# Kernel optimization log

Hardware: AMD Instinct MI355X
Metric: run time of the kernel (lower is better)

## Reference

```python
import jax, jax.numpy as jnp
import numpy as np

N_LVL = 127.0   # 8-bit symmetric: 2**(8-1) - 1
BN_EPS = 1e-5
PATCH = 16


def quant_act(x):
    """Per-tensor 8-bit symmetric quant-dequant (HAWQ-style QuantAct, dynamic range)."""
    scale = jnp.max(jnp.abs(x)) / N_LVL
    xq = jnp.clip(jnp.round(x / scale), -N_LVL, N_LVL) * scale
    return xq, scale


def setup_inputs() -> dict:
    key = jax.random.key(0)
    k0, k1, k2, k3, k4 = jax.random.split(key, 5)
    B, C, H = 128, 3, 224
    dim = 768
    x = jax.random.normal(k0, (B, C, H, H), jnp.float32)
    W = jax.random.normal(k1, (dim, C, PATCH, PATCH), jnp.float32) * 0.02
    b = jax.random.normal(k2, (dim,), jnp.float32) * 0.02
    gamma = jnp.ones((dim,), jnp.float32)
    beta = jnp.zeros((dim,), jnp.float32)
    run_mean = jax.random.normal(k3, (dim,), jnp.float32) * 0.1
    run_var = jax.random.uniform(k4, (dim,), jnp.float32, 0.5, 1.5)
    return {"x": x, "W": W, "b": b, "gamma": gamma, "beta": beta,
            "run_mean": run_mean, "run_var": run_var}


def reference(x, W, b, gamma, beta, run_mean, run_var):
    # --- quant_input ---
    x_q, pre_s = quant_act(x)                                   # [B,3,224,224], scalar
    # --- QuantConv2d: per-out-channel 8-bit symmetric weight quant ---
    w_scale = jnp.max(jnp.abs(W), axis=(1, 2, 3), keepdims=True) / N_LVL  # [dim,1,1,1]
    w_int = jnp.round(W / w_scale)
    x_int = x_q / pre_s                                         # integer-valued activations
    comb_s = w_scale[:, 0, 0, 0] * pre_s                        # [dim] conv output scale
    b_int = jnp.round(b / comb_s)
    y = jax.lax.conv_general_dilated(
        x_int, w_int, window_strides=(PATCH, PATCH), padding='VALID',
        dimension_numbers=('NCHW', 'OIHW', 'NCHW'))             # [B,768,14,14]
    y = (y + b_int[None, :, None, None]) * comb_s[None, :, None, None]
    # --- quant_act_conv ---
    y, _ = quant_act(y)
    # --- GELU (torch nn.GELU default: exact erf) ---
    y = jax.nn.gelu(y, approximate=False)
    # --- qact1 ---
    y, _ = quant_act(y)
    # --- BatchNorm2d (eval mode, running stats) ---
    inv = gamma / jnp.sqrt(run_var + BN_EPS)
    y = y * inv[None, :, None, None] + (beta - run_mean * inv)[None, :, None, None]
    # --- qact2 ---
    y, act_scale = quant_act(y)
    return y, act_scale
```

## Files before the change

### kernel.cpp

```cpp
#include <hip/hip_runtime.h>

#define TOT   19267584
#define MROWS 25088
#define KD    768
#define NPB   196
#define CHW   150528

typedef unsigned int uint;
typedef __attribute__((ext_vector_type(4))) int i32x4;

#define OFF_AQ   0ull
#define OFF_WQ   19267584ull
#define OFF_WSC  19857408ull
#define OFF_INV  19860480ull
#define OFF_SHF  19863552ull
#define OFF_PA   19866624ull
#define OFF_PB   19871328ull
#define OFF_CMN  19876032ull
#define OFF_CMX  19879104ull

__device__ __forceinline__ float wave_max(float v) {
#pragma unroll
  for (int off = 32; off > 0; off >>= 1) v = fmaxf(v, __shfl_xor(v, off));
  return v;
}

__device__ __forceinline__ float block_max(float v) {
  __shared__ float red[4];
  v = wave_max(v);
  __syncthreads();
  if ((threadIdx.x & 63) == 0) red[threadIdx.x >> 6] = v;
  __syncthreads();
  return fmaxf(fmaxf(red[0], red[1]), fmaxf(red[2], red[3]));
}

__global__ void k_maxabs(const float* __restrict__ x, float* __restrict__ pA) {
  const int i0 = blockIdx.x * 256 + threadIdx.x;
  const float4* x4 = (const float4*)x;
  float m = 0.f;
#pragma unroll
  for (int j = 0; j < 16; j += 4) {
    float4 a = x4[i0 + (j + 0) * 301056];
    float4 b = x4[i0 + (j + 1) * 301056];
    float4 c = x4[i0 + (j + 2) * 301056];
    float4 d = x4[i0 + (j + 3) * 301056];
    m = fmaxf(m, fmaxf(fmaxf(fabsf(a.x), fabsf(a.y)), fmaxf(fabsf(a.z), fabsf(a.w))));
    m = fmaxf(m, fmaxf(fmaxf(fabsf(b.x), fabsf(b.y)), fmaxf(fabsf(b.z), fabsf(b.w))));
    m = fmaxf(m, fmaxf(fmaxf(fabsf(c.x), fabsf(c.y)), fmaxf(fabsf(c.z), fabsf(c.w))));
    m = fmaxf(m, fmaxf(fmaxf(fabsf(d.x), fabsf(d.y)), fmaxf(fabsf(d.z), fabsf(d.w))));
  }
  float bm = block_max(m);
  if (threadIdx.x == 0) pA[blockIdx.x] = bm;
}

__global__ void k_wquant(const float* __restrict__ W, const float* __restrict__ gamma,
                         const float* __restrict__ beta, const float* __restrict__ rmean,
                         const float* __restrict__ rvar, signed char* __restrict__ wq,
                         float* __restrict__ wscale, float* __restrict__ inv_,
                         float* __restrict__ shf) {
  const int oc = blockIdx.x;
  const float* row = W + oc * KD;
  float m = 0.f;
  for (int k = threadIdx.x; k < KD; k += 256) m = fmaxf(m, fabsf(row[k]));
  const float ws_ = block_max(m) / 127.0f;
  for (int k = threadIdx.x; k < KD; k += 256)
    wq[oc * KD + k] = (signed char)(int)rintf(row[k] / ws_);
  if (threadIdx.x == 0) {
    wscale[oc] = ws_;
    float iv = gamma[oc] / sqrtf(rvar[oc] + 1e-5f);
    inv_[oc] = iv;
    shf[oc] = __fsub_rn(beta[oc], __fmul_rn(rmean[oc], iv));
  }
}

__global__ void k_im2col(const float* __restrict__ x, const float* __restrict__ pA,
                         signed char* __restrict__ aq) {
  float mm = 0.f;
  for (int i = threadIdx.x; i < 1176; i += 256) mm = fmaxf(mm, pA[i]);
  const float ps = block_max(mm) / 127.0f;
  const int u = blockIdx.x * 256 + threadIdx.x;
  const int p = u / 48, r = u - p * 48;
  const int c = r >> 4, kh = r & 15;
  const int b = p / NPB, pp = p - b * NPB;
  const int ph = pp / 14, pw = pp - ph * 14;
  const float* src = x + (((b * 3 + c) * 224 + ph * 16 + kh) * 224 + pw * 16);
  float4 v0 = *(const float4*)(src);
  float4 v1 = *(const float4*)(src + 4);
  float4 v2 = *(const float4*)(src + 8);
  float4 v3 = *(const float4*)(src + 12);
#define Q8(v) ((int)fminf(fmaxf(rintf((v) / ps), -127.f), 127.f) & 255)
  uint4 o;
  o.x = Q8(v0.x) | (Q8(v0.y) << 8) | (Q8(v0.z) << 16) | ((uint)Q8(v0.w) << 24);
  o.y = Q8(v1.x) | (Q8(v1.y) << 8) | (Q8(v1.z) << 16) | ((uint)Q8(v1.w) << 24);
  o.z = Q8(v2.x) | (Q8(v2.y) << 8) | (Q8(v2.z) << 16) | ((uint)Q8(v2.w) << 24);
  o.w = Q8(v3.x) | (Q8(v3.y) << 8) | (Q8(v3.z) << 16) | ((uint)Q8(v3.w) << 24);
#undef Q8
  *(uint4*)(aq + (size_t)p * KD + (r << 4)) = o;
}

__device__ __forceinline__ void gl_lds16(const void* g, void* l) {
  __builtin_amdgcn_global_load_lds((const __attribute__((address_space(1))) void*)g,
                                   (__attribute__((address_space(3))) void*)l, 16, 0, 0);
}

__global__ __launch_bounds__(256) void k_gemm(const signed char* __restrict__ aq,
                                              const signed char* __restrict__ wq,
                                              const float* __restrict__ bias,
                                              const float* __restrict__ wscale,
                                              const float* __restrict__ pA,
                                              float* __restrict__ y,
                                              float* __restrict__ pB) {
  __shared__ __align__(16) signed char lA[3][8192];
  __shared__ __align__(16) signed char lB[3][8192];
  const int tid = threadIdx.x, lane = tid & 63, wv = tid >> 6;
  const int bsw = (blockIdx.x & 7) * 147 + (blockIdx.x >> 3);
  const int bm = bsw / 6, bn = bsw - 6 * (bsw / 6);
  const int wr = wv >> 1, wc = wv & 1;

  const int ci0 = wv * 2, ci1 = wv * 2 + 1;
  const int rr0 = ci0 * 16 + (lane >> 2);
  const int rr1 = ci1 * 16 + (lane >> 2);
  const int bo = (((lane & 3) ^ ((lane >> 3) & 3)) << 4);
  const signed char* gA0 = aq + (size_t)(bm * 128 + rr0) * KD + bo;
  const signed char* gA1 = aq + (size_t)(bm * 128 + rr1) * KD + bo;
  const signed char* gB0 = wq + (size_t)(bn * 128 + rr0) * KD + bo;
  const signed char* gB1 = wq + (size_t)(bn * 128 + rr1) * KD + bo;

  i32x4 acc[4][4];
#pragma unroll
  for (int m = 0; m < 4; ++m)
#pragma unroll
    for (int n = 0; n < 4; ++n) acc[m][n] = (i32x4){0, 0, 0, 0};

  const int rbase = lane & 15;
  const int kg = (((lane >> 4) << 4)) ^ (((lane >> 1) & 3) << 4);

#define STAGE(T, B)                                   \
  {                                                   \
    const int kk_ = (T) * 64;                         \
    gl_lds16(gA0 + kk_, &lA[B][ci0 * 1024]);          \
    gl_lds16(gA1 + kk_, &lA[B][ci1 * 1024]);          \
    gl_lds16(gB0 + kk_, &lB[B][ci0 * 1024]);          \
    gl_lds16(gB1 + kk_, &lB[B][ci1 * 1024]);          \
  }

  STAGE(0, 0)
  STAGE(1, 1)
#pragma unroll
  for (int t = 0; t < 12; ++t) {
    if (t < 11) { asm volatile("s_waitcnt vmcnt(4)" ::: "memory"); }
    else        { asm volatile("s_waitcnt vmcnt(0)" ::: "memory"); }
    __builtin_amdgcn_s_barrier();
    __builtin_amdgcn_sched_barrier(0);
    const int b = t % 3;
    i32x4 af[4], bfr[4];
#pragma unroll
    for (int m = 0; m < 4; ++m)
      af[m] = *(const i32x4*)&lA[b][(wr * 64 + m * 16 + rbase) * 64 + kg];
#pragma unroll
    for (int n = 0; n < 4; ++n)
      bfr[n] = *(const i32x4*)&lB[b][(wc * 64 + n * 16 + rbase) * 64 + kg];
    if (t < 10) STAGE(t + 2, (t + 2) % 3)
#pragma unroll
    for (int m = 0; m < 4; ++m)
#pragma unroll
      for (int n = 0; n < 4; ++n)
        acc[m][n] = __builtin_amdgcn_mfma_i32_16x16x64_i8(af[m], bfr[n], acc[m][n], 0, 0, 0);
  }
#undef STAGE

  float mm = 0.f;
  for (int i = tid; i < 1176; i += 256) mm = fmaxf(mm, pA[i]);
  const float ps = block_max(mm) / 127.0f;

  float lmax = 0.f;
  const int prow = (lane >> 4) << 2;
#pragma unroll
  for (int n = 0; n < 4; ++n) {
    const int oc = bn * 128 + wc * 64 + n * 16 + rbase;
    const float comb = wscale[oc] * ps;
    const float bint = rintf(bias[oc] / comb);
#pragma unroll
    for (int m = 0; m < 4; ++m) {
      const int p0 = bm * 128 + wr * 64 + m * 16 + prow;
      const int img = p0 / 196;
      const int q = p0 - img * 196;
      float4 o;
      o.x = ((float)acc[m][n][0] + bint) * comb;
      o.y = ((float)acc[m][n][1] + bint) * comb;
      o.z = ((float)acc[m][n][2] + bint) * comb;
      o.w = ((float)acc[m][n][3] + bint) * comb;
      lmax = fmaxf(lmax, fmaxf(fmaxf(fabsf(o.x), fabsf(o.y)), fmaxf(fabsf(o.z), fabsf(o.w))));
      *(float4*)(y + (size_t)img * CHW + (size_t)oc * 196 + q) = o;
    }
  }
  float bm_ = block_max(lmax);
  if (tid == 0) pB[blockIdx.x] = bm_;
}

__global__ void k_gelu_chan(const float* __restrict__ y, const float* __restrict__ pB,
                            signed char* __restrict__ k1, float* __restrict__ chmn,
                            float* __restrict__ chmx) {
  const int c = blockIdx.x;
  float mm = 0.f;
  for (int i = threadIdx.x; i < 1176; i += 256) mm = fmaxf(mm, pB[i]);
  const float s1 = block_max(mm) / 127.0f;
  __shared__ float tab[255];
  for (int t = threadIdx.x; t < 255; t += 256) {
    float y1 = (float)(t - 127) * s1;
    float e = erff(y1 * 0.70710678118654752f);
    tab[t] = (y1 * (e + 1.0f)) * 0.5f;
  }
  __syncthreads();
  float mn = 1e30f, mx = -1e30f;
  const float4* y4 = (const float4*)y;
  char4* k4 = (char4*)k1;
#define ADDR(u) ((size_t)((u) / 49) * (CHW / 4) + (size_t)c * 49 + ((u) - ((u) / 49) * 49))
#define PROC(v, a4)                                                        \
  {                                                                        \
    int ia = (int)fminf(fmaxf(rintf((v).x / s1), -127.f), 127.f);          \
    int ib = (int)fminf(fmaxf(rintf((v).y / s1), -127.f), 127.f);          \
    int ic = (int)fminf(fmaxf(rintf((v).z / s1), -127.f), 127.f);          \
    int id = (int)fminf(fmaxf(rintf((v).w / s1), -127.f), 127.f);          \
    char4 kk;                                                              \
    kk.x = (signed char)ia; kk.y = (signed char)ib;                        \
    kk.z = (signed char)ic; kk.w = (signed char)id;                        \
    k4[a4] = kk;                                                           \
    float ga = tab[ia + 127], gb = tab[ib + 127];                          \
    float gc = tab[ic + 127], gd = tab[id + 127];                          \
    mn = fminf(mn, fminf(fminf(ga, gb), fminf(gc, gd)));                   \
    mx = fmaxf(mx, fmaxf(fmaxf(ga, gb), fmaxf(gc, gd)));                   \
  }
  for (int r = 0; r < 6; ++r) {
    const int u0 = threadIdx.x + r * 1024;
    const size_t a0 = ADDR(u0), a1 = ADDR(u0 + 256), a2 = ADDR(u0 + 512), a3 = ADDR(u0 + 768);
    float4 v0 = y4[a0];
    float4 v1 = y4[a1];
    float4 v2 = y4[a2];
    float4 v3 = y4[a3];
    PROC(v0, a0) PROC(v1, a1) PROC(v2, a2) PROC(v3, a3)
  }
  if (threadIdx.x < 128) {
    const int u = 6144 + threadIdx.x;
    const size_t a = ADDR(u);
    float4 v = y4[a];
    PROC(v, a)
  }
#undef PROC
#undef ADDR
  __shared__ float rmn[4], rmx[4];
#pragma unroll
  for (int off = 32; off > 0; off >>= 1) {
    mn = fminf(mn, __shfl_xor(mn, off));
    mx = fmaxf(mx, __shfl_xor(mx, off));
  }
  const int lane = threadIdx.x & 63, wvx = threadIdx.x >> 6;
  if (lane == 0) { rmn[wvx] = mn; rmx[wvx] = mx; }
  __syncthreads();
  if (threadIdx.x == 0) {
    chmn[c] = fminf(fminf(rmn[0], rmn[1]), fminf(rmn[2], rmn[3]));
    chmx[c] = fmaxf(fmaxf(rmx[0], rmx[1]), fmaxf(rmx[2], rmx[3]));
  }
}

__global__ void k_final(const signed char* __restrict__ k1, const float* __restrict__ pB,
                        const float* __restrict__ chmn, const float* __restrict__ chmx,
                        const float* __restrict__ inv_, const float* __restrict__ shf,
                        float* __restrict__ out) {
  float mm = 0.f;
  for (int i = threadIdx.x; i < 1176; i += 256) mm = fmaxf(mm, pB[i]);
  const float s1 = block_max(mm) / 127.0f;
  float m2 = 0.f;
  for (int c = threadIdx.x; c < 768; c += 256)
    m2 = fmaxf(m2, fmaxf(fabsf(chmn[c]), fabsf(chmx[c])));
  const float s2 = block_max(m2) / 127.0f;
  float m4 = 0.f;
  for (int c = threadIdx.x; c < 768; c += 256) {
    float iv = inv_[c], sh = shf[c];
    float a = fminf(fmaxf(rintf(chmn[c] / s2), -127.f), 127.f) * s2;
    float b = fminf(fmaxf(rintf(chmx[c] / s2), -127.f), 127.f) * s2;
    float ya = __fadd_rn(__fmul_rn(a, iv), sh);
    float yb = __fadd_rn(__fmul_rn(b, iv), sh);
    m4 = fmaxf(m4, fmaxf(fabsf(ya), fabsf(yb)));
  }
  const float s3 = block_max(m4) / 127.0f;

  __shared__ float tab[255];
  for (int t = threadIdx.x; t < 255; t += 256) {
    float y1 = (float)(t - 127) * s1;
    float e = erff(y1 * 0.70710678118654752f);
    float y2 = (y1 * (e + 1.0f)) * 0.5f;
    float q2 = fminf(fmaxf(rintf(y2 / s2), -127.f), 127.f);
    tab[t] = q2 * s2;
  }
  __syncthreads();
  const int i = blockIdx.x * 256 + threadIdx.x;
  const char4* k4 = (const char4*)k1;
  char4 a0 = k4[i];
  char4 a1 = k4[i + 1204224];
  char4 a2 = k4[i + 2 * 1204224];
  char4 a3 = k4[i + 3 * 1204224];
  float4* out4 = (float4*)out;
#define FIN(kk, idx)                                                       \
  {                                                                        \
    int c = ((idx) / 49) % 768;                                            \
    float iv = inv_[c], sh = shf[c];                                       \
    float fa = __fadd_rn(__fmul_rn(tab[kk.x + 127], iv), sh);              \
    float fb = __fadd_rn(__fmul_rn(tab[kk.y + 127], iv), sh);              \
    float fc = __fadd_rn(__fmul_rn(tab[kk.z + 127], iv), sh);              \
    float fd = __fadd_rn(__fmul_rn(tab[kk.w + 127], iv), sh);              \
    float4 o;                                                              \
    o.x = fminf(fmaxf(rintf(fa / s3), -127.f), 127.f) * s3;                \
    o.y = fminf(fmaxf(rintf(fb / s3), -127.f), 127.f) * s3;                \
    o.z = fminf(fmaxf(rintf(fc / s3), -127.f), 127.f) * s3;                \
    o.w = fminf(fmaxf(rintf(fd / s3), -127.f), 127.f) * s3;                \
    out4[idx] = o;                                                         \
  }
  FIN(a0, i)
  FIN(a1, i + 1204224)
  FIN(a2, i + 2 * 1204224)
  FIN(a3, i + 3 * 1204224)
#undef FIN
  if (blockIdx.x == 0 && threadIdx.x == 0) out[TOT] = s3;
}

extern "C" void kernel_launch(void* const* d_in, const int* in_sizes, int n_in,
                              void* d_out, int out_size, void* d_ws, size_t ws_size,
                              hipStream_t stream) {
  const float* x     = (const float*)d_in[0];
  const float* W     = (const float*)d_in[1];
  const float* bias  = (const float*)d_in[2];
  const float* gamma = (const float*)d_in[3];
  const float* beta  = (const float*)d_in[4];
  const float* rmean = (const float*)d_in[5];
  const float* rvar  = (const float*)d_in[6];
  float* out = (float*)d_out;
  char* ws = (char*)d_ws;

  signed char* aq  = (signed char*)(ws + OFF_AQ);
  signed char* wq  = (signed char*)(ws + OFF_WQ);
  float* wsc  = (float*)(ws + OFF_WSC);
  float* inv_ = (float*)(ws + OFF_INV);
  float* shf  = (float*)(ws + OFF_SHF);
  float* pA   = (float*)(ws + OFF_PA);
  float* pB   = (float*)(ws + OFF_PB);
  float* cmn  = (float*)(ws + OFF_CMN);
  float* cmx  = (float*)(ws + OFF_CMX);
  signed char* k1 = (signed char*)(ws + OFF_AQ);

  k_maxabs<<<1176, 256, 0, stream>>>(x, pA);
  k_wquant<<<768, 256, 0, stream>>>(W, gamma, beta, rmean, rvar, wq, wsc, inv_, shf);
  k_im2col<<<4704, 256, 0, stream>>>(x, pA, aq);
  k_gemm<<<1176, 256, 0, stream>>>(aq, wq, bias, wsc, pA, out, pB);
  k_gelu_chan<<<768, 256, 0, stream>>>(out, pB, k1, cmn, cmx);
  k_final<<<4704, 256, 0, stream>>>(k1, pB, cmn, cmx, inv_, shf, out);
}
```

Baseline: 125.6 us.

## Tile GEMM operands, store GEMM output row-major, split channel reductions into stages

```diff
diff --git a/kernel.cpp b/kernel.cpp
--- a/kernel.cpp
+++ b/kernel.cpp
@@ -16,8 +16,11 @@
 #define OFF_SHF  19863552ull
 #define OFF_PA   19866624ull
 #define OFF_PB   19871328ull
-#define OFF_CMN  19876032ull
-#define OFF_CMX  19879104ull
+#define OFF_SC   19876032ull
+#define OFF_CMN  19880736ull
+#define OFF_CMX  19883808ull
+#define OFF_PMN  19886880ull
+#define OFF_PMX  24703776ull
 
 __device__ __forceinline__ float wave_max(float v) {
 #pragma unroll
@@ -34,42 +37,47 @@
   return fmaxf(fmaxf(red[0], red[1]), fmaxf(red[2], red[3]));
 }
 
-__global__ void k_maxabs(const float* __restrict__ x, float* __restrict__ pA) {
-  const int i0 = blockIdx.x * 256 + threadIdx.x;
-  const float4* x4 = (const float4*)x;
-  float m = 0.f;
-#pragma unroll
-  for (int j = 0; j < 16; j += 4) {
-    float4 a = x4[i0 + (j + 0) * 301056];
-    float4 b = x4[i0 + (j + 1) * 301056];
-    float4 c = x4[i0 + (j + 2) * 301056];
-    float4 d = x4[i0 + (j + 3) * 301056];
-    m = fmaxf(m, fmaxf(fmaxf(fabsf(a.x), fabsf(a.y)), fmaxf(fabsf(a.z), fabsf(a.w))));
-    m = fmaxf(m, fmaxf(fmaxf(fabsf(b.x), fabsf(b.y)), fmaxf(fabsf(b.z), fabsf(b.w))));
-    m = fmaxf(m, fmaxf(fmaxf(fabsf(c.x), fabsf(c.y)), fmaxf(fabsf(c.z), fabsf(c.w))));
-    m = fmaxf(m, fmaxf(fmaxf(fabsf(d.x), fabsf(d.y)), fmaxf(fabsf(d.z), fabsf(d.w))));
-  }
-  float bm = block_max(m);
-  if (threadIdx.x == 0) pA[blockIdx.x] = bm;
-}
-
-__global__ void k_wquant(const float* __restrict__ W, const float* __restrict__ gamma,
+__device__ __forceinline__ size_t tiled_addr(int row, int k) {
+  return (size_t)(row >> 7) * 98304 + (size_t)(k >> 6) * 8192 + ((row & 127) << 6) + (k & 63);
+}
+
+__global__ void k_max_wq(const float* __restrict__ x, float* __restrict__ pA,
+                         const float* __restrict__ W, const float* __restrict__ gamma,
                          const float* __restrict__ beta, const float* __restrict__ rmean,
                          const float* __restrict__ rvar, signed char* __restrict__ wq,
                          float* __restrict__ wscale, float* __restrict__ inv_,
                          float* __restrict__ shf) {
-  const int oc = blockIdx.x;
-  const float* row = W + oc * KD;
-  float m = 0.f;
-  for (int k = threadIdx.x; k < KD; k += 256) m = fmaxf(m, fabsf(row[k]));
-  const float ws_ = block_max(m) / 127.0f;
-  for (int k = threadIdx.x; k < KD; k += 256)
-    wq[oc * KD + k] = (signed char)(int)rintf(row[k] / ws_);
-  if (threadIdx.x == 0) {
-    wscale[oc] = ws_;
-    float iv = gamma[oc] / sqrtf(rvar[oc] + 1e-5f);
-    inv_[oc] = iv;
-    shf[oc] = __fsub_rn(beta[oc], __fmul_rn(rmean[oc], iv));
+  if (blockIdx.x < 1176) {
+    const int i0 = blockIdx.x * 256 + threadIdx.x;
+    const float4* x4 = (const float4*)x;
+    float m = 0.f;
+#pragma unroll
+    for (int j = 0; j < 16; j += 4) {
+      float4 a = x4[i0 + (j + 0) * 301056];
+      float4 b = x4[i0 + (j + 1) * 301056];
+      float4 c = x4[i0 + (j + 2) * 301056];
+      float4 d = x4[i0 + (j + 3) * 301056];
+      m = fmaxf(m, fmaxf(fmaxf(fabsf(a.x), fabsf(a.y)), fmaxf(fabsf(a.z), fabsf(a.w))));
+      m = fmaxf(m, fmaxf(fmaxf(fabsf(b.x), fabsf(b.y)), fmaxf(fabsf(b.z), fabsf(b.w))));
+      m = fmaxf(m, fmaxf(fmaxf(fabsf(c.x), fabsf(c.y)), fmaxf(fabsf(c.z), fabsf(c.w))));
+      m = fmaxf(m, fmaxf(fmaxf(fabsf(d.x), fabsf(d.y)), fmaxf(fabsf(d.z), fabsf(d.w))));
+    }
+    float bm = block_max(m);
+    if (threadIdx.x == 0) pA[blockIdx.x] = bm;
+  } else {
+    const int oc = blockIdx.x - 1176;
+    const float* row = W + oc * KD;
+    float m = 0.f;
+    for (int k = threadIdx.x; k < KD; k += 256) m = fmaxf(m, fabsf(row[k]));
+    const float ws_ = block_max(m) / 127.0f;
+    for (int k = threadIdx.x; k < KD; k += 256)
+      wq[tiled_addr(oc, k)] = (signed char)(int)rintf(row[k] / ws_);
+    if (threadIdx.x == 0) {
+      wscale[oc] = ws_;
+      float iv = gamma[oc] / sqrtf(rvar[oc] + 1e-5f);
+      inv_[oc] = iv;
+      shf[oc] = __fsub_rn(beta[oc], __fmul_rn(rmean[oc], iv));
+    }
   }
 }
 
@@ -95,7 +103,8 @@
   o.z = Q8(v2.x) | (Q8(v2.y) << 8) | (Q8(v2.z) << 16) | ((uint)Q8(v2.w) << 24);
   o.w = Q8(v3.x) | (Q8(v3.y) << 8) | (Q8(v3.z) << 16) | ((uint)Q8(v3.w) << 24);
 #undef Q8
-  *(uint4*)(aq + (size_t)p * KD + (r << 4)) = o;
+  *(uint4*)(aq + (size_t)(p >> 7) * 98304 + (size_t)(r >> 2) * 8192 + ((p & 127) << 6) +
+            ((r & 3) << 4)) = o;
 }
 
 __device__ __forceinline__ void gl_lds16(const void* g, void* l) {
@@ -110,21 +119,23 @@
                                               const float* __restrict__ pA,
                                               float* __restrict__ y,
                                               float* __restrict__ pB) {
-  __shared__ __align__(16) signed char lA[3][8192];
-  __shared__ __align__(16) signed char lB[3][8192];
+  __shared__ __align__(16) signed char lA[2][8192];
+  __shared__ __align__(16) signed char lB[2][8192];
   const int tid = threadIdx.x, lane = tid & 63, wv = tid >> 6;
   const int bsw = (blockIdx.x & 7) * 147 + (blockIdx.x >> 3);
   const int bm = bsw / 6, bn = bsw - 6 * (bsw / 6);
   const int wr = wv >> 1, wc = wv & 1;
 
+  float mm = 0.f;
+  for (int i = tid; i < 1176; i += 256) mm = fmaxf(mm, pA[i]);
+  const float ps_ = block_max(mm) / 127.0f;
+
   const int ci0 = wv * 2, ci1 = wv * 2 + 1;
-  const int rr0 = ci0 * 16 + (lane >> 2);
-  const int rr1 = ci1 * 16 + (lane >> 2);
-  const int bo = (((lane & 3) ^ ((lane >> 3) & 3)) << 4);
-  const signed char* gA0 = aq + (size_t)(bm * 128 + rr0) * KD + bo;
-  const signed char* gA1 = aq + (size_t)(bm * 128 + rr1) * KD + bo;
-  const signed char* gB0 = wq + (size_t)(bn * 128 + rr0) * KD + bo;
-  const signed char* gB1 = wq + (size_t)(bn * 128 + rr1) * KD + bo;
+  const int lo = ((lane >> 2) << 6) + (((lane & 3) ^ ((lane >> 3) & 3)) << 4);
+  const signed char* gA0 = aq + (size_t)bm * 98304 + ci0 * 1024 + lo;
+  const signed char* gA1 = aq + (size_t)bm * 98304 + ci1 * 1024 + lo;
+  const signed char* gB0 = wq + (size_t)bn * 98304 + ci0 * 1024 + lo;
+  const signed char* gB1 = wq + (size_t)bn * 98304 + ci1 * 1024 + lo;
 
   i32x4 acc[4][4];
 #pragma unroll
@@ -133,11 +144,11 @@
     for (int n = 0; n < 4; ++n) acc[m][n] = (i32x4){0, 0, 0, 0};
 
   const int rbase = lane & 15;
-  const int kg = (((lane >> 4) << 4)) ^ (((lane >> 1) & 3) << 4);
+  const int kg = ((lane >> 4) << 4) ^ (((lane >> 1) & 3) << 4);
 
 #define STAGE(T, B)                                   \
   {                                                   \
-    const int kk_ = (T) * 64;                         \
+    const size_t kk_ = (size_t)(T) * 8192;            \
     gl_lds16(gA0 + kk_, &lA[B][ci0 * 1024]);          \
     gl_lds16(gA1 + kk_, &lA[B][ci1 * 1024]);          \
     gl_lds16(gB0 + kk_, &lB[B][ci0 * 1024]);          \
@@ -145,182 +156,178 @@
   }
 
   STAGE(0, 0)
-  STAGE(1, 1)
-#pragma unroll
+  __syncthreads();
+
+  int cur = 0;
   for (int t = 0; t < 12; ++t) {
-    if (t < 11) { asm volatile("s_waitcnt vmcnt(4)" ::: "memory"); }
-    else        { asm volatile("s_waitcnt vmcnt(0)" ::: "memory"); }
-    __builtin_amdgcn_s_barrier();
-    __builtin_amdgcn_sched_barrier(0);
-    const int b = t % 3;
+    if (t < 11) STAGE(t + 1, cur ^ 1)
     i32x4 af[4], bfr[4];
 #pragma unroll
     for (int m = 0; m < 4; ++m)
-      af[m] = *(const i32x4*)&lA[b][(wr * 64 + m * 16 + rbase) * 64 + kg];
+      af[m] = *(const i32x4*)&lA[cur][(wr * 64 + m * 16 + rbase) * 64 + kg];
 #pragma unroll
     for (int n = 0; n < 4; ++n)
-      bfr[n] = *(const i32x4*)&lB[b][(wc * 64 + n * 16 + rbase) * 64 + kg];
-    if (t < 10) STAGE(t + 2, (t + 2) % 3)
+      bfr[n] = *(const i32x4*)&lB[cur][(wc * 64 + n * 16 + rbase) * 64 + kg];
 #pragma unroll
     for (int m = 0; m < 4; ++m)
 #pragma unroll
       for (int n = 0; n < 4; ++n)
-        acc[m][n] = __builtin_amdgcn_mfma_i32_16x16x64_i8(af[m], bfr[n], acc[m][n], 0, 0, 0);
+        acc[m][n] = __builtin_amdgcn_mfma_i32_16x16x64_i8(bfr[n], af[m], acc[m][n], 0, 0, 0);
+    __syncthreads();
+    cur ^= 1;
   }
 #undef STAGE
 
-  float mm = 0.f;
-  for (int i = tid; i < 1176; i += 256) mm = fmaxf(mm, pA[i]);
-  const float ps = block_max(mm) / 127.0f;
-
   float lmax = 0.f;
-  const int prow = (lane >> 4) << 2;
 #pragma unroll
   for (int n = 0; n < 4; ++n) {
-    const int oc = bn * 128 + wc * 64 + n * 16 + rbase;
-    const float comb = wscale[oc] * ps;
-    const float bint = rintf(bias[oc] / comb);
+    const int ocb = bn * 128 + wc * 64 + n * 16 + ((lane >> 4) << 2);
+    const float4 ws4 = *(const float4*)&wscale[ocb];
+    const float4 b4 = *(const float4*)&bias[ocb];
+    const float c0 = ws4.x * ps_, c1 = ws4.y * ps_, c2 = ws4.z * ps_, c3 = ws4.w * ps_;
+    const float i0 = rintf(b4.x / c0), i1 = rintf(b4.y / c1);
+    const float i2 = rintf(b4.z / c2), i3 = rintf(b4.w / c3);
 #pragma unroll
     for (int m = 0; m < 4; ++m) {
-      const int p0 = bm * 128 + wr * 64 + m * 16 + prow;
-      const int img = p0 / 196;
-      const int q = p0 - img * 196;
+      const int p = bm * 128 + wr * 64 + m * 16 + rbase;
       float4 o;
-      o.x = ((float)acc[m][n][0] + bint) * comb;
-      o.y = ((float)acc[m][n][1] + bint) * comb;
-      o.z = ((float)acc[m][n][2] + bint) * comb;
-      o.w = ((float)acc[m][n][3] + bint) * comb;
+      o.x = ((float)acc[m][n][0] + i0) * c0;
+      o.y = ((float)acc[m][n][1] + i1) * c1;
+      o.z = ((float)acc[m][n][2] + i2) * c2;
+      o.w = ((float)acc[m][n][3] + i3) * c3;
       lmax = fmaxf(lmax, fmaxf(fmaxf(fabsf(o.x), fabsf(o.y)), fmaxf(fabsf(o.z), fabsf(o.w))));
-      *(float4*)(y + (size_t)img * CHW + (size_t)oc * 196 + q) = o;
+      *(float4*)(y + (size_t)p * 768 + ocb) = o;
     }
   }
   float bm_ = block_max(lmax);
   if (tid == 0) pB[blockIdx.x] = bm_;
 }
 
-__global__ void k_gelu_chan(const float* __restrict__ y, const float* __restrict__ pB,
-                            signed char* __restrict__ k1, float* __restrict__ chmn,
-                            float* __restrict__ chmx) {
-  const int c = blockIdx.x;
+__global__ void k_gelu(const float* __restrict__ y, const float* __restrict__ pB,
+                       signed char* __restrict__ k1, float* __restrict__ pmn,
+                       float* __restrict__ pmx) {
+  const int b = blockIdx.x;
+  const int t = threadIdx.x;
   float mm = 0.f;
-  for (int i = threadIdx.x; i < 1176; i += 256) mm = fmaxf(mm, pB[i]);
+  for (int i = t; i < 1176; i += 256) mm = fmaxf(mm, pB[i]);
   const float s1 = block_max(mm) / 127.0f;
   __shared__ float tab[255];
-  for (int t = threadIdx.x; t < 255; t += 256) {
-    float y1 = (float)(t - 127) * s1;
+  for (int i = t; i < 255; i += 256) {
+    float y1 = (float)(i - 127) * s1;
     float e = erff(y1 * 0.70710678118654752f);
-    tab[t] = (y1 * (e + 1.0f)) * 0.5f;
-  }
-  __syncthreads();
-  float mn = 1e30f, mx = -1e30f;
-  const float4* y4 = (const float4*)y;
-  char4* k4 = (char4*)k1;
-#define ADDR(u) ((size_t)((u) / 49) * (CHW / 4) + (size_t)c * 49 + ((u) - ((u) / 49) * 49))
-#define PROC(v, a4)                                                        \
-  {                                                                        \
-    int ia = (int)fminf(fmaxf(rintf((v).x / s1), -127.f), 127.f);          \
-    int ib = (int)fminf(fmaxf(rintf((v).y / s1), -127.f), 127.f);          \
-    int ic = (int)fminf(fmaxf(rintf((v).z / s1), -127.f), 127.f);          \
-    int id = (int)fminf(fmaxf(rintf((v).w / s1), -127.f), 127.f);          \
-    char4 kk;                                                              \
-    kk.x = (signed char)ia; kk.y = (signed char)ib;                        \
-    kk.z = (signed char)ic; kk.w = (signed char)id;                        \
-    k4[a4] = kk;                                                           \
-    float ga = tab[ia + 127], gb = tab[ib + 127];                          \
-    float gc = tab[ic + 127], gd = tab[id + 127];                          \
-    mn = fminf(mn, fminf(fminf(ga, gb), fminf(gc, gd)));                   \
-    mx = fmaxf(mx, fmaxf(fmaxf(ga, gb), fmaxf(gc, gd)));                   \
-  }
-  for (int r = 0; r < 6; ++r) {
-    const int u0 = threadIdx.x + r * 1024;
-    const size_t a0 = ADDR(u0), a1 = ADDR(u0 + 256), a2 = ADDR(u0 + 512), a3 = ADDR(u0 + 768);
-    float4 v0 = y4[a0];
-    float4 v1 = y4[a1];
-    float4 v2 = y4[a2];
-    float4 v3 = y4[a3];
-    PROC(v0, a0) PROC(v1, a1) PROC(v2, a2) PROC(v3, a3)
-  }
-  if (threadIdx.x < 128) {
-    const int u = 6144 + threadIdx.x;
-    const size_t a = ADDR(u);
-    float4 v = y4[a];
-    PROC(v, a)
-  }
-#undef PROC
-#undef ADDR
-  __shared__ float rmn[4], rmx[4];
-#pragma unroll
-  for (int off = 32; off > 0; off >>= 1) {
-    mn = fminf(mn, __shfl_xor(mn, off));
-    mx = fmaxf(mx, __shfl_xor(mx, off));
-  }
-  const int lane = threadIdx.x & 63, wvx = threadIdx.x >> 6;
-  if (lane == 0) { rmn[wvx] = mn; rmx[wvx] = mx; }
-  __syncthreads();
-  if (threadIdx.x == 0) {
-    chmn[c] = fminf(fminf(rmn[0], rmn[1]), fminf(rmn[2], rmn[3]));
-    chmx[c] = fmaxf(fmaxf(rmx[0], rmx[1]), fmaxf(rmx[2], rmx[3]));
-  }
-}
-
-__global__ void k_final(const signed char* __restrict__ k1, const float* __restrict__ pB,
-                        const float* __restrict__ chmn, const float* __restrict__ chmx,
-                        const float* __restrict__ inv_, const float* __restrict__ shf,
-                        float* __restrict__ out) {
-  float mm = 0.f;
-  for (int i = threadIdx.x; i < 1176; i += 256) mm = fmaxf(mm, pB[i]);
-  const float s1 = block_max(mm) / 127.0f;
+    tab[i] = (y1 * (e + 1.0f)) * 0.5f;
+  }
+  __syncthreads();
+  float mn0 = 1e30f, mx0 = -1e30f, mn1 = 1e30f, mx1 = -1e30f, mn2 = 1e30f, mx2 = -1e30f;
+  const float* yb = y + (size_t)b * 16 * 768 + t;
+  signed char* kb = k1 + (size_t)b * 16 * 768 + t;
+#pragma unroll 4
+  for (int row = 0; row < 16; ++row) {
+    const float* yr = yb + row * 768;
+    float v0 = yr[0], v1 = yr[256], v2 = yr[512];
+    int a = (int)fminf(fmaxf(rintf(v0 / s1), -127.f), 127.f);
+    int bq = (int)fminf(fmaxf(rintf(v1 / s1), -127.f), 127.f);
+    int cq = (int)fminf(fmaxf(rintf(v2 / s1), -127.f), 127.f);
+    signed char* kr = kb + row * 768;
+    kr[0] = (signed char)a;
+    kr[256] = (signed char)bq;
+    kr[512] = (signed char)cq;
+    float g0 = tab[a + 127], g1 = tab[bq + 127], g2 = tab[cq + 127];
+    mn0 = fminf(mn0, g0); mx0 = fmaxf(mx0, g0);
+    mn1 = fminf(mn1, g1); mx1 = fmaxf(mx1, g1);
+    mn2 = fminf(mn2, g2); mx2 = fmaxf(mx2, g2);
+  }
+  pmn[(size_t)t * 1568 + b] = mn0;         pmx[(size_t)t * 1568 + b] = mx0;
+  pmn[(size_t)(t + 256) * 1568 + b] = mn1; pmx[(size_t)(t + 256) * 1568 + b] = mx1;
+  pmn[(size_t)(t + 512) * 1568 + b] = mn2; pmx[(size_t)(t + 512) * 1568 + b] = mx2;
+}
+
+__global__ void k_chred(const float* __restrict__ pmn, const float* __restrict__ pmx,
+                        float* __restrict__ cmn, float* __restrict__ cmx) {
+  const int c = blockIdx.x;
+  float lo = 1e30f, hi = -1e30f;
+  for (int i = threadIdx.x; i < 1568; i += 256) {
+    lo = fminf(lo, pmn[(size_t)c * 1568 + i]);
+    hi = fmaxf(hi, pmx[(size_t)c * 1568 + i]);
+  }
+  float bhi = block_max(hi);
+  float blo = -block_max(-lo);
+  if (threadIdx.x == 0) { cmn[c] = blo; cmx[c] = bhi; }
+}
+
+__global__ void k_scales(const float* __restrict__ pB, const float* __restrict__ cmn,
+                         const float* __restrict__ cmx, const float* __restrict__ inv_,
+                         const float* __restrict__ shf, uint* __restrict__ sc) {
+  const int t = threadIdx.x;
+  float m = 0.f;
+  for (int i = t; i < 1176; i += 256) m = fmaxf(m, pB[i]);
+  const float s1 = block_max(m) / 127.0f;
   float m2 = 0.f;
-  for (int c = threadIdx.x; c < 768; c += 256)
-    m2 = fmaxf(m2, fmaxf(fabsf(chmn[c]), fabsf(chmx[c])));
+  for (int c = t; c < 768; c += 256)
+    m2 = fmaxf(m2, fmaxf(fabsf(cmn[c]), fabsf(cmx[c])));
   const float s2 = block_max(m2) / 127.0f;
   float m4 = 0.f;
-  for (int c = threadIdx.x; c < 768; c += 256) {
+  for (int c = t; c < 768; c += 256) {
     float iv = inv_[c], sh = shf[c];
-    float a = fminf(fmaxf(rintf(chmn[c] / s2), -127.f), 127.f) * s2;
-    float b = fminf(fmaxf(rintf(chmx[c] / s2), -127.f), 127.f) * s2;
+    float a = fminf(fmaxf(rintf(cmn[c] / s2), -127.f), 127.f) * s2;
+    float b = fminf(fmaxf(rintf(cmx[c] / s2), -127.f), 127.f) * s2;
     float ya = __fadd_rn(__fmul_rn(a, iv), sh);
     float yb = __fadd_rn(__fmul_rn(b, iv), sh);
     m4 = fmaxf(m4, fmaxf(fabsf(ya), fabsf(yb)));
   }
   const float s3 = block_max(m4) / 127.0f;
-
+  if (t == 0) {
+    sc[0] = __float_as_uint(s1);
+    sc[1] = __float_as_uint(s2);
+    sc[2] = __float_as_uint(s3);
+  }
+}
+
+__global__ void k_final(const signed char* __restrict__ k1, const uint* __restrict__ sc,
+                        const float* __restrict__ inv_, const float* __restrict__ shf,
+                        float* __restrict__ out) {
+  const float s1 = __uint_as_float(sc[0]);
+  const float s2 = __uint_as_float(sc[1]);
+  const float s3 = __uint_as_float(sc[2]);
   __shared__ float tab[255];
-  for (int t = threadIdx.x; t < 255; t += 256) {
-    float y1 = (float)(t - 127) * s1;
+  for (int i = threadIdx.x; i < 255; i += 256) {
+    float y1 = (float)(i - 127) * s1;
     float e = erff(y1 * 0.70710678118654752f);
     float y2 = (y1 * (e + 1.0f)) * 0.5f;
     float q2 = fminf(fmaxf(rintf(y2 / s2), -127.f), 127.f);
-    tab[t] = q2 * s2;
-  }
-  __syncthreads();
-  const int i = blockIdx.x * 256 + threadIdx.x;
-  const char4* k4 = (const char4*)k1;
-  char4 a0 = k4[i];
-  char4 a1 = k4[i + 1204224];
-  char4 a2 = k4[i + 2 * 1204224];
-  char4 a3 = k4[i + 3 * 1204224];
-  float4* out4 = (float4*)out;
-#define FIN(kk, idx)                                                       \
-  {                                                                        \
-    int c = ((idx) / 49) % 768;                                            \
-    float iv = inv_[c], sh = shf[c];                                       \
-    float fa = __fadd_rn(__fmul_rn(tab[kk.x + 127], iv), sh);              \
-    float fb = __fadd_rn(__fmul_rn(tab[kk.y + 127], iv), sh);              \
-    float fc = __fadd_rn(__fmul_rn(tab[kk.z + 127], iv), sh);              \
-    float fd = __fadd_rn(__fmul_rn(tab[kk.w + 127], iv), sh);              \
-    float4 o;                                                              \
-    o.x = fminf(fmaxf(rintf(fa / s3), -127.f), 127.f) * s3;                \
-    o.y = fminf(fmaxf(rintf(fb / s3), -127.f), 127.f) * s3;                \
-    o.z = fminf(fmaxf(rintf(fc / s3), -127.f), 127.f) * s3;                \
-    o.w = fminf(fmaxf(rintf(fd / s3), -127.f), 127.f) * s3;                \
-    out4[idx] = o;                                                         \
-  }
-  FIN(a0, i)
-  FIN(a1, i + 1204224)
-  FIN(a2, i + 2 * 1204224)
-  FIN(a3, i + 3 * 1204224)
-#undef FIN
+    tab[i] = q2 * s2;
+  }
+  __syncthreads();
+  const int img = blockIdx.x / 12, ocg = blockIdx.x - 12 * (blockIdx.x / 12);
+  const int oc0 = ocg * 64;
+  const int g = threadIdx.x & 15;
+  const signed char* kbase = k1 + (size_t)img * 196 * 768;
+  float* obase = out + (size_t)img * CHW;
+#define FIN4(Q, OC, IV, SH)                                                  \
+  {                                                                          \
+    const signed char* kp = kbase + (size_t)(Q)*768 + (OC);                  \
+    int a = kp[0], b = kp[768], c = kp[1536], d = kp[2304];                  \
+    float fa = __fadd_rn(__fmul_rn(tab[a + 127], (IV)), (SH));               \
+    float fb = __fadd_rn(__fmul_rn(tab[b + 127], (IV)), (SH));               \
+    float fc = __fadd_rn(__fmul_rn(tab[c + 127], (IV)), (SH));               \
+    float fd = __fadd_rn(__fmul_rn(tab[d + 127], (IV)), (SH));               \
+    float4 o;                                                                \
+    o.x = fminf(fmaxf(rintf(fa / s3), -127.f), 127.f) * s3;                  \
+    o.y = fminf(fmaxf(rintf(fb / s3), -127.f), 127.f) * s3;                  \
+    o.z = fminf(fmaxf(rintf(fc / s3), -127.f), 127.f) * s3;                  \
+    o.w = fminf(fmaxf(rintf(fd / s3), -127.f), 127.f) * s3;                  \
+    *(float4*)(obase + (size_t)(OC)*196 + (Q)) = o;                          \
+  }
+#pragma unroll
+  for (int ocs = 0; ocs < 4; ++ocs) {
+    const int oc = oc0 + ocs * 16 + (threadIdx.x >> 4);
+    const float iv = inv_[oc], sh = shf[oc];
+    FIN4(g * 4, oc, iv, sh)
+    FIN4(64 + g * 4, oc, iv, sh)
+    FIN4(128 + g * 4, oc, iv, sh)
+    if (g == 0) FIN4(192, oc, iv, sh)
+  }
+#undef FIN4
   if (blockIdx.x == 0 && threadIdx.x == 0) out[TOT] = s3;
 }
 
@@ -344,14 +351,18 @@
   float* shf  = (float*)(ws + OFF_SHF);
   float* pA   = (float*)(ws + OFF_PA);
   float* pB   = (float*)(ws + OFF_PB);
+  uint*  sc   = (uint*)(ws + OFF_SC);
   float* cmn  = (float*)(ws + OFF_CMN);
   float* cmx  = (float*)(ws + OFF_CMX);
+  float* pmn  = (float*)(ws + OFF_PMN);
+  float* pmx  = (float*)(ws + OFF_PMX);
   signed char* k1 = (signed char*)(ws + OFF_AQ);
 
-  k_maxabs<<<1176, 256, 0, stream>>>(x, pA);
-  k_wquant<<<768, 256, 0, stream>>>(W, gamma, beta, rmean, rvar, wq, wsc, inv_, shf);
+  k_max_wq<<<1944, 256, 0, stream>>>(x, pA, W, gamma, beta, rmean, rvar, wq, wsc, inv_, shf);
   k_im2col<<<4704, 256, 0, stream>>>(x, pA, aq);
   k_gemm<<<1176, 256, 0, stream>>>(aq, wq, bias, wsc, pA, out, pB);
-  k_gelu_chan<<<768, 256, 0, stream>>>(out, pB, k1, cmn, cmx);
-  k_final<<<4704, 256, 0, stream>>>(k1, pB, cmn, cmx, inv_, shf, out);
-}
+  k_gelu<<<1568, 256, 0, stream>>>(out, pB, k1, pmn, pmx);
+  k_chred<<<768, 256, 0, stream>>>(pmn, pmx, cmn, cmx);
+  k_scales<<<1, 256, 0, stream>>>(pB, cmn, cmx, inv_, shf, sc);
+  k_final<<<1536, 256, 0, stream>>>(k1, sc, inv_, shf, out);
+}
```

New measurement: 163.6 us. 30.2% more time.
